# Kernel optimization log

Measured on AMD Instinct MI355X. Metric: run time of the kernel, lower is better.

## Reference

```python
import jax, jax.numpy as jnp
import numpy as np

B, T, C = 2, 4096, 768
NH = 12
HD = C // NH  # 64


def setup_inputs() -> dict:
    key = jax.random.key(0)
    k0, k1, k2, k3, k4 = jax.random.split(key, 5)
    x = jax.random.normal(k0, (B, T, C), dtype=jnp.float32)
    # parameters (stored as [in, out] for x @ W)
    w_attn = jax.random.normal(k1, (C, 3 * C), dtype=jnp.float32) * 0.02
    b_attn = jnp.zeros((3 * C,), dtype=jnp.float32)
    w_proj = jax.random.normal(k2, (C, C), dtype=jnp.float32) * 0.02
    b_proj = jnp.zeros((C,), dtype=jnp.float32)
    return {"x": x, "w_attn": w_attn, "b_attn": b_attn, "w_proj": w_proj, "b_proj": b_proj}


def reference(x, w_attn, b_attn, w_proj, b_proj):
    Bv, Tv, Cv = x.shape
    qkv = x @ w_attn + b_attn  # (B,T,3C)
    q, k, v = jnp.split(qkv, 3, axis=2)
    # (B, NH, T, HD)
    q = q.reshape(Bv, Tv, NH, HD).transpose(0, 2, 1, 3)
    k = k.reshape(Bv, Tv, NH, HD).transpose(0, 2, 1, 3)
    v = v.reshape(Bv, Tv, NH, HD).transpose(0, 2, 1, 3)
    att = jnp.einsum('bhqd,bhkd->bhqk', q, k) / jnp.sqrt(jnp.float32(HD))
    causal = jnp.tril(jnp.ones((Tv, Tv), dtype=bool))  # mask buffer slice
    att = jnp.where(causal[None, None, :, :], att, jnp.float32(-jnp.inf))
    att = jax.nn.softmax(att, axis=-1)
    y = jnp.einsum('bhqk,bhkd->bhqd', att, v)
    y = y.transpose(0, 2, 1, 3).reshape(Bv, Tv, Cv)
    y = y @ w_proj + b_proj
    return y
```

## Files before the change

### kernel.cpp

```cpp
#include <hip/hip_runtime.h>

typedef __bf16 bf16;
typedef float f32x4 __attribute__((ext_vector_type(4)));
typedef bf16 bf16x8v __attribute__((ext_vector_type(8)));
typedef bf16 bf16x4v __attribute__((ext_vector_type(4)));

#define MFMA_BF16(a, b, c) __builtin_amdgcn_mfma_f32_16x16x32_bf16((a), (b), (c), 0, 0, 0)

__device__ __forceinline__ void async16(const bf16* g, bf16* l) {
  __builtin_amdgcn_global_load_lds(
      (const __attribute__((address_space(1))) void*)g,
      (__attribute__((address_space(3))) void*)l, 16, 0, 0);
}

__global__ __launch_bounds__(256) void convert_kernel(
    const float* __restrict__ in, bf16* __restrict__ out, int n8) {
  int i = blockIdx.x * 256 + threadIdx.x;
  if (i >= n8) return;
  const float4* p = (const float4*)in + (size_t)i * 2;
  float4 a = p[0], b = p[1];
  bf16x8v o;
  o[0] = (bf16)a.x; o[1] = (bf16)a.y; o[2] = (bf16)a.z; o[3] = (bf16)a.w;
  o[4] = (bf16)b.x; o[5] = (bf16)b.y; o[6] = (bf16)b.z; o[7] = (bf16)b.w;
  ((bf16x8v*)out)[i] = o;
}

__global__ __launch_bounds__(256) void transpose_conv_kernel(
    const float* __restrict__ in, bf16* __restrict__ out, int R, int Ccols) {
  __shared__ float tile[32][33];
  int c0 = blockIdx.x * 32, r0 = blockIdx.y * 32;
  int tx = threadIdx.x & 31;
  int ty = threadIdx.x >> 5;
#pragma unroll
  for (int i = 0; i < 4; ++i) {
    int r = ty + i * 8;
    tile[r][tx] = in[(size_t)(r0 + r) * Ccols + c0 + tx];
  }
  __syncthreads();
#pragma unroll
  for (int i = 0; i < 4; ++i) {
    int c = ty + i * 8;
    out[(size_t)(c0 + c) * R + r0 + tx] = (bf16)tile[tx][c];
  }
}

__global__ __launch_bounds__(256) void transpose_bf16_kernel(
    const bf16* __restrict__ in, bf16* __restrict__ out, int R, int Ccols) {
  __shared__ bf16 tile[32][33];
  const bf16* inp = in + (size_t)blockIdx.z * R * Ccols;
  bf16* outp = out + (size_t)blockIdx.z * R * Ccols;
  int c0 = blockIdx.x * 32, r0 = blockIdx.y * 32;
  int tx = threadIdx.x & 31;
  int ty = threadIdx.x >> 5;
#pragma unroll
  for (int i = 0; i < 4; ++i) {
    int r = ty + i * 8;
    tile[r][tx] = inp[(size_t)(r0 + r) * Ccols + c0 + tx];
  }
  __syncthreads();
#pragma unroll
  for (int i = 0; i < 4; ++i) {
    int c = ty + i * 8;
    outp[(size_t)(c0 + c) * R + r0 + tx] = tile[tx][c];
  }
}

template <int MODE>
__global__ __launch_bounds__(256) void gemm_kernel(
    const bf16* __restrict__ A, const bf16* __restrict__ Bt,
    const float* __restrict__ bias, int N, float* __restrict__ outf,
    bf16* __restrict__ qo, bf16* __restrict__ ko, bf16* __restrict__ vo) {
  constexpr int Kdim = 768;
  __shared__ __align__(16) bf16 As[128][32];
  __shared__ __align__(16) bf16 Bs[128][32];
  const int tid = threadIdx.x;
  const int lane = tid & 63;
  const int wave = tid >> 6;
  const int wm = (wave >> 1) * 64, wn = (wave & 1) * 64;
  const int m0 = blockIdx.y * 128, n0 = blockIdx.x * 128;
  const int l15 = lane & 15, q4 = lane >> 4;

  f32x4 acc[4][4] = {};

  const int ca = wave * 2;
  const int ar = lane >> 2;
  const int ac = (lane & 3) * 8;
  bf16* asBase = &As[0][0];
  bf16* bsBase = &Bs[0][0];

  for (int k0 = 0; k0 < Kdim; k0 += 32) {
    const bf16* gA = A + (size_t)(m0 + ca * 16 + ar) * Kdim + k0 + ac;
    async16(gA, asBase + ca * 512);
    async16(gA + 16 * Kdim, asBase + (ca + 1) * 512);
    const bf16* gB = Bt + (size_t)(n0 + ca * 16 + ar) * Kdim + k0 + ac;
    async16(gB, bsBase + ca * 512);
    async16(gB + 16 * Kdim, bsBase + (ca + 1) * 512);
    __syncthreads();
    bf16x8v af[4], bfg[4];
#pragma unroll
    for (int i = 0; i < 4; ++i)
      af[i] = *(const bf16x8v*)&As[wm + i * 16 + l15][q4 * 8];
#pragma unroll
    for (int i = 0; i < 4; ++i)
      bfg[i] = *(const bf16x8v*)&Bs[wn + i * 16 + l15][q4 * 8];
#pragma unroll
    for (int mi = 0; mi < 4; ++mi)
#pragma unroll
      for (int ni = 0; ni < 4; ++ni)
        acc[mi][ni] = MFMA_BF16(af[mi], bfg[ni], acc[mi][ni]);
    __syncthreads();
  }

#pragma unroll
  for (int mi = 0; mi < 4; ++mi) {
#pragma unroll
    for (int ni = 0; ni < 4; ++ni) {
      int col = n0 + wn + ni * 16 + l15;
      float bv = bias[col];
#pragma unroll
      for (int r = 0; r < 4; ++r) {
        int row = m0 + wm + mi * 16 + q4 * 4 + r;
        float val = acc[mi][ni][r] + bv;
        if (MODE == 0) {
          outf[(size_t)row * N + col] = val;
        } else {
          int sel = col / 768;
          int cc = col - sel * 768;
          int h = cc >> 6, d = cc & 63;
          int b = row >> 12, t = row & 4095;
          bf16* dst = sel == 0 ? qo : (sel == 1 ? ko : vo);
          dst[((size_t)(b * 12 + h) * 4096 + t) * 64 + d] = (bf16)val;
        }
      }
    }
  }
}

__global__ __launch_bounds__(512, 6) void attn_kernel(
    const bf16* __restrict__ q, const bf16* __restrict__ k,
    const bf16* __restrict__ vt, bf16* __restrict__ y) {
  __shared__ __align__(16) bf16 Kb[2][64][64];
  __shared__ __align__(16) bf16 Vb[2][64][64];
  __shared__ __align__(16) bf16 Ps[8][16][64];
  const int tid = threadIdx.x;
  const int lane = tid & 63, wave = tid >> 6;
  const int l15 = lane & 15, q4 = lane >> 4;
  const int swz = l15 & 7;
  const int id = blockIdx.x;
  const int bh = id % 24;
  const int p = id / 24;
  const int rs = (wave < 4) ? ((63 - p) * 64 + wave * 16)
                            : (p * 64 + (wave - 4) * 16);
  const int hb = bh % 12, bb = bh / 12;

  const int gr = lane >> 3;
  const int sj = (lane & 7) ^ gr;
  const bf16* kgbase = k + (size_t)bh * 4096 * 64;
  const bf16* vgbase = vt + (size_t)bh * 64 * 4096;

  bf16x8v ones;
#pragma unroll
  for (int j = 0; j < 8; ++j) ones[j] = (bf16)1.0f;

  bf16x8v qf[2];
  {
    const bf16* qrow = q + ((size_t)bh * 4096 + rs + l15) * 64 + q4 * 8;
#pragma unroll
    for (int ks = 0; ks < 2; ++ks) {
      bf16x8v t8 = *(const bf16x8v*)(qrow + ks * 32);
#pragma unroll
      for (int j = 0; j < 8; ++j) t8[j] = (bf16)((float)t8[j] * 0.18033688f);
      qf[ks] = t8;
    }
  }

  f32x4 o[4] = {};
  f32x4 ol = {};

  auto stage = [&](int kt, int buf) {
    const int t0k = kt * 64;
    async16(kgbase + (size_t)(t0k + wave * 8 + gr) * 64 + sj * 8,
            &Kb[buf][wave * 8][0]);
    async16(vgbase + (size_t)(wave * 8 + gr) * 4096 + t0k + sj * 8,
            &Vb[buf][wave * 8][0]);
  };

  auto sm_full = [&](f32x4 (&s)[4]) {
#pragma unroll
    for (int ni = 0; ni < 4; ++ni)
#pragma unroll
      for (int r = 0; r < 4; ++r)
        s[ni][r] = __builtin_amdgcn_exp2f(s[ni][r] - 28.8539008f);
  };
  auto sm_mask = [&](f32x4 (&s)[4], int lim) {
#pragma unroll
    for (int ni = 0; ni < 4; ++ni)
#pragma unroll
      for (int r = 0; r < 4; ++r)
        s[ni][r] = (ni * 16 + q4 * 4 + r <= lim)
                       ? __builtin_amdgcn_exp2f(s[ni][r] - 28.8539008f)
                       : 0.0f;
  };
  auto pwrite = [&](const f32x4 (&s)[4]) {
#pragma unroll
    for (int ni = 0; ni < 4; ++ni) {
      bf16x4v pv4;
#pragma unroll
      for (int e = 0; e < 4; ++e) pv4[e] = (bf16)s[ni][e];
      const int jb = ni * 2 + (q4 >> 1);
      *(bf16x4v*)&Ps[wave][l15][((jb ^ (l15 & 7)) * 8) + (q4 & 1) * 4] = pv4;
    }
  };

  const int ktmax = 64 - p;
  stage(0, 0);

  for (int kt = 0; kt < ktmax; ++kt) {
    const int buf = kt & 1;
    __syncthreads();
    if (kt + 1 < ktmax) stage(kt + 1, buf ^ 1);
    const int t0 = kt * 64;

    if (t0 <= rs + 15) {
      f32x4 s[4] = {};
      __builtin_amdgcn_s_setprio(1);
#pragma unroll
      for (int ni = 0; ni < 4; ++ni) {
#pragma unroll
        for (int ks = 0; ks < 2; ++ks) {
          bf16x8v kf = *(const bf16x8v*)&Kb[buf][ni * 16 + l15]
                                           [((ks * 4 + q4) ^ swz) * 8];
          s[ni] = MFMA_BF16(kf, qf[ks], s[ni]);
        }
      }
      __builtin_amdgcn_s_setprio(0);

      if (t0 + 63 <= rs) sm_full(s); else sm_mask(s, rs + l15 - t0);
      pwrite(s);

      bf16x8v pf[2];
#pragma unroll
      for (int ks = 0; ks < 2; ++ks)
        pf[ks] = *(const bf16x8v*)&Ps[wave][l15][((ks * 4 + q4) ^ swz) * 8];

      __builtin_amdgcn_s_setprio(1);
#pragma unroll
      for (int d4 = 0; d4 < 4; ++d4) {
#pragma unroll
        for (int ks = 0; ks < 2; ++ks) {
          bf16x8v vf = *(const bf16x8v*)&Vb[buf][d4 * 16 + l15]
                                           [((ks * 4 + q4) ^ swz) * 8];
          o[d4] = MFMA_BF16(pf[ks], vf, o[d4]);
        }
      }
#pragma unroll
      for (int ks = 0; ks < 2; ++ks) ol = MFMA_BF16(pf[ks], ones, ol);
      __builtin_amdgcn_s_setprio(0);
    }
  }

#pragma unroll
  for (int d4 = 0; d4 < 4; ++d4)
#pragma unroll
    for (int r = 0; r < 4; ++r) {
      int row = rs + q4 * 4 + r;
      y[((size_t)(bb * 4096 + row)) * 768 + hb * 64 + d4 * 16 + l15] =
          (bf16)(o[d4][r] / ol[r]);
    }
}

extern "C" void kernel_launch(void* const* d_in, const int* in_sizes, int n_in,
                              void* d_out, int out_size, void* d_ws,
                              size_t ws_size, hipStream_t stream) {
  const float* x = (const float*)d_in[0];
  const float* w_attn = (const float*)d_in[1];
  const float* b_attn = (const float*)d_in[2];
  const float* w_proj = (const float*)d_in[3];
  const float* b_proj = (const float*)d_in[4];
  float* out = (float*)d_out;

  char* ws = (char*)d_ws;
  size_t off = 0;
  auto carve = [&](size_t elems) {
    char* p = ws + off;
    off += ((elems * sizeof(bf16) + 255) & ~(size_t)255);
    return (bf16*)p;
  };
  bf16* xb = carve((size_t)8192 * 768);
  bf16* wt_attn = carve((size_t)2304 * 768);
  bf16* wt_proj = carve((size_t)768 * 768);
  bf16* qb = carve((size_t)24 * 4096 * 64);
  bf16* kb = carve((size_t)24 * 4096 * 64);
  bf16* vb = carve((size_t)24 * 4096 * 64);
  bf16* vtb = xb;
  bf16* yb = vb;

  convert_kernel<<<(8192 * 768 / 8 + 255) / 256, 256, 0, stream>>>(
      x, xb, 8192 * 768 / 8);
  transpose_conv_kernel<<<dim3(2304 / 32, 768 / 32), 256, 0, stream>>>(
      w_attn, wt_attn, 768, 2304);
  transpose_conv_kernel<<<dim3(768 / 32, 768 / 32), 256, 0, stream>>>(
      w_proj, wt_proj, 768, 768);
  gemm_kernel<1><<<dim3(2304 / 128, 8192 / 128), 256, 0, stream>>>(
      xb, wt_attn, b_attn, 2304, nullptr, qb, kb, vb);
  transpose_bf16_kernel<<<dim3(64 / 32, 4096 / 32, 24), 256, 0, stream>>>(
      vb, vtb, 4096, 64);
  attn_kernel<<<dim3(768), 512, 0, stream>>>(qb, kb, vtb, yb);
  gemm_kernel<0><<<dim3(768 / 128, 8192 / 128), 256, 0, stream>>>(
      yb, wt_proj, b_proj, 768, out, nullptr, nullptr, nullptr);
}
```

Measured before the change: 242.1 us.

## Fuse prep kernels and double GEMM K-tile with XOR-swizzled LDS layout

```diff
diff --git a/kernel.cpp b/kernel.cpp
--- a/kernel.cpp
+++ b/kernel.cpp
@@ -13,24 +13,35 @@
       (__attribute__((address_space(3))) void*)l, 16, 0, 0);
 }
 
-__global__ __launch_bounds__(256) void convert_kernel(
-    const float* __restrict__ in, bf16* __restrict__ out, int n8) {
-  int i = blockIdx.x * 256 + threadIdx.x;
-  if (i >= n8) return;
-  const float4* p = (const float4*)in + (size_t)i * 2;
-  float4 a = p[0], b = p[1];
-  bf16x8v o;
-  o[0] = (bf16)a.x; o[1] = (bf16)a.y; o[2] = (bf16)a.z; o[3] = (bf16)a.w;
-  o[4] = (bf16)b.x; o[5] = (bf16)b.y; o[6] = (bf16)b.z; o[7] = (bf16)b.w;
-  ((bf16x8v*)out)[i] = o;
-}
-
-__global__ __launch_bounds__(256) void transpose_conv_kernel(
-    const float* __restrict__ in, bf16* __restrict__ out, int R, int Ccols) {
+__global__ __launch_bounds__(256) void prep_kernel(
+    const float* __restrict__ x, bf16* __restrict__ xb,
+    const float* __restrict__ w_attn, bf16* __restrict__ wt_attn,
+    const float* __restrict__ w_proj, bf16* __restrict__ wt_proj) {
   __shared__ float tile[32][33];
-  int c0 = blockIdx.x * 32, r0 = blockIdx.y * 32;
-  int tx = threadIdx.x & 31;
-  int ty = threadIdx.x >> 5;
+  const int b = blockIdx.x;
+  if (b < 3072) {
+    int i = b * 256 + threadIdx.x;
+    const float4* p = (const float4*)x + (size_t)i * 2;
+    float4 a = p[0], c = p[1];
+    bf16x8v o;
+    o[0] = (bf16)a.x; o[1] = (bf16)a.y; o[2] = (bf16)a.z; o[3] = (bf16)a.w;
+    o[4] = (bf16)c.x; o[5] = (bf16)c.y; o[6] = (bf16)c.z; o[7] = (bf16)c.w;
+    ((bf16x8v*)xb)[i] = o;
+    return;
+  }
+  const float* in;
+  bf16* out;
+  int Ccols, bidx;
+  if (b < 4800) {
+    in = w_attn; out = wt_attn; Ccols = 2304; bidx = b - 3072;
+  } else {
+    in = w_proj; out = wt_proj; Ccols = 768; bidx = b - 4800;
+  }
+  const int R = 768;
+  const int gx = Ccols / 32;
+  const int c0 = (bidx % gx) * 32, r0 = (bidx / gx) * 32;
+  const int tx = threadIdx.x & 31;
+  const int ty = threadIdx.x >> 5;
 #pragma unroll
   for (int i = 0; i < 4; ++i) {
     int r = ty + i * 8;
@@ -71,43 +82,46 @@
     const float* __restrict__ bias, int N, float* __restrict__ outf,
     bf16* __restrict__ qo, bf16* __restrict__ ko, bf16* __restrict__ vo) {
   constexpr int Kdim = 768;
-  __shared__ __align__(16) bf16 As[128][32];
-  __shared__ __align__(16) bf16 Bs[128][32];
+  __shared__ __align__(16) bf16 As[128][64];
+  __shared__ __align__(16) bf16 Bs[128][64];
   const int tid = threadIdx.x;
   const int lane = tid & 63;
   const int wave = tid >> 6;
   const int wm = (wave >> 1) * 64, wn = (wave & 1) * 64;
   const int m0 = blockIdx.y * 128, n0 = blockIdx.x * 128;
   const int l15 = lane & 15, q4 = lane >> 4;
+  const int swz = l15 & 7;
 
   f32x4 acc[4][4] = {};
 
-  const int ca = wave * 2;
-  const int ar = lane >> 2;
-  const int ac = (lane & 3) * 8;
-  bf16* asBase = &As[0][0];
-  bf16* bsBase = &Bs[0][0];
-
-  for (int k0 = 0; k0 < Kdim; k0 += 32) {
-    const bf16* gA = A + (size_t)(m0 + ca * 16 + ar) * Kdim + k0 + ac;
-    async16(gA, asBase + ca * 512);
-    async16(gA + 16 * Kdim, asBase + (ca + 1) * 512);
-    const bf16* gB = Bt + (size_t)(n0 + ca * 16 + ar) * Kdim + k0 + ac;
-    async16(gB, bsBase + ca * 512);
-    async16(gB + 16 * Kdim, bsBase + (ca + 1) * 512);
+  const int gr = lane >> 3;
+  const int sj = (lane & 7) ^ gr;
+
+  for (int k0 = 0; k0 < Kdim; k0 += 64) {
+#pragma unroll
+    for (int c = 0; c < 4; ++c) {
+      const int r0 = wave * 32 + c * 8;
+      async16(A + (size_t)(m0 + r0 + gr) * Kdim + k0 + sj * 8, &As[r0][0]);
+      async16(Bt + (size_t)(n0 + r0 + gr) * Kdim + k0 + sj * 8, &Bs[r0][0]);
+    }
     __syncthreads();
-    bf16x8v af[4], bfg[4];
-#pragma unroll
-    for (int i = 0; i < 4; ++i)
-      af[i] = *(const bf16x8v*)&As[wm + i * 16 + l15][q4 * 8];
-#pragma unroll
-    for (int i = 0; i < 4; ++i)
-      bfg[i] = *(const bf16x8v*)&Bs[wn + i * 16 + l15][q4 * 8];
-#pragma unroll
-    for (int mi = 0; mi < 4; ++mi)
-#pragma unroll
-      for (int ni = 0; ni < 4; ++ni)
-        acc[mi][ni] = MFMA_BF16(af[mi], bfg[ni], acc[mi][ni]);
+#pragma unroll
+    for (int ks = 0; ks < 2; ++ks) {
+      bf16x8v af[4], bfg[4];
+#pragma unroll
+      for (int i = 0; i < 4; ++i)
+        af[i] =
+            *(const bf16x8v*)&As[wm + i * 16 + l15][((ks * 4 + q4) ^ swz) * 8];
+#pragma unroll
+      for (int i = 0; i < 4; ++i)
+        bfg[i] =
+            *(const bf16x8v*)&Bs[wn + i * 16 + l15][((ks * 4 + q4) ^ swz) * 8];
+#pragma unroll
+      for (int mi = 0; mi < 4; ++mi)
+#pragma unroll
+        for (int ni = 0; ni < 4; ++ni)
+          acc[mi][ni] = MFMA_BF16(af[mi], bfg[ni], acc[mi][ni]);
+    }
     __syncthreads();
   }
 
@@ -295,12 +309,8 @@
   bf16* vtb = xb;
   bf16* yb = vb;
 
-  convert_kernel<<<(8192 * 768 / 8 + 255) / 256, 256, 0, stream>>>(
-      x, xb, 8192 * 768 / 8);
-  transpose_conv_kernel<<<dim3(2304 / 32, 768 / 32), 256, 0, stream>>>(
-      w_attn, wt_attn, 768, 2304);
-  transpose_conv_kernel<<<dim3(768 / 32, 768 / 32), 256, 0, stream>>>(
-      w_proj, wt_proj, 768, 768);
+  prep_kernel<<<5376, 256, 0, stream>>>(x, xb, w_attn, wt_attn, w_proj,
+                                        wt_proj);
   gemm_kernel<1><<<dim3(2304 / 128, 8192 / 128), 256, 0, stream>>>(
       xb, wt_attn, b_attn, 2304, nullptr, qb, kb, vb);
   transpose_bf16_kernel<<<dim3(64 / 32, 4096 / 32, 24), 256, 0, stream>>>(
```

Measured after the change: 236.6 us. 2.2% less time.
